# Optimization experiments

Measured on AMD Instinct MI355X. Metric: run time of the kernel, lower is better.

Reference implementation:

```python
import jax, jax.numpy as jnp
import numpy as np

NODE_DIM = 128
DEPTH = 4
N_NODES = 10000
N_EDGES = 320000


def setup_inputs() -> dict:
    key = jax.random.key(0)
    ks = jax.random.split(key, 12)
    s = 0.05
    D = NODE_DIM
    inp = {
        'h': jax.random.normal(ks[0], (N_NODES, D), jnp.float32),
        'x': jax.random.normal(ks[1], (N_NODES, 3), jnp.float32),
        'edges': jax.random.randint(ks[2], (2, N_EDGES), 0, N_NODES, jnp.int32),
        # edge_mlp: Linear(2D+1 -> D), SiLU, Linear(D -> D), SiLU  (per layer)
        'edge_w1': jax.random.normal(ks[3], (DEPTH, 2 * D + 1, D), jnp.float32) * s,
        'edge_b1': jnp.zeros((DEPTH, D), jnp.float32),
        'edge_w2': jax.random.normal(ks[4], (DEPTH, D, D), jnp.float32) * s,
        'edge_b2': jnp.zeros((DEPTH, D), jnp.float32),
        # node_mlp: Linear(2D -> D), SiLU, Linear(D -> D)  (per layer)
        'node_w1': jax.random.normal(ks[5], (DEPTH, 2 * D, D), jnp.float32) * s,
        'node_b1': jnp.zeros((DEPTH, D), jnp.float32),
        'node_w2': jax.random.normal(ks[6], (DEPTH, D, D), jnp.float32) * s,
        'node_b2': jnp.zeros((DEPTH, D), jnp.float32),
        # coord_mlp (only used by last layer, update_coords=True):
        # Linear(D -> D), SiLU, Linear(D -> 1, bias=False)
        'coord_w1': jax.random.normal(ks[7], (D, D), jnp.float32) * s,
        'coord_b1': jnp.zeros((D,), jnp.float32),
        'coord_w2': jax.random.normal(ks[8], (D, 1), jnp.float32) * s,
    }
    return inp


def reference(h, x, edges, edge_w1, edge_b1, edge_w2, edge_b2,
              node_w1, node_b1, node_w2, node_b2,
              coord_w1, coord_b1, coord_w2):
    silu = jax.nn.silu
    row, col = edges[0], edges[1]
    n = h.shape[0]
    for i in range(DEPTH):
        # coord2radial
        coord_diff = x[row] - x[col]                       # [E, 3]
        radial = jnp.sum(coord_diff * coord_diff, axis=-1, keepdims=True)  # [E, 1]
        # edge_model: m_ij = edge_mlp([h_i, h_j, radial])
        feat = jnp.concatenate([h[row], h[col], radial], axis=-1)  # [E, 2D+1]
        m = silu(feat @ edge_w1[i] + edge_b1[i])
        m = silu(m @ edge_w2[i] + edge_b2[i])              # [E, D]
        # coord_model (only last layer, coords_agg='mean')
        if i == DEPTH - 1:
            w = silu(m @ coord_w1 + coord_b1) @ coord_w2   # [E, 1]
            trans = coord_diff * w                          # [E, 3]
            agg = jax.ops.segment_sum(trans, row, num_segments=n)
            cnt = jax.ops.segment_sum(jnp.ones((row.shape[0], 1), trans.dtype),
                                      row, num_segments=n)
            x = x + agg / jnp.maximum(cnt, 1.0)
        # node_model: h = h + node_mlp([h, sum_j m_ij])  (residual=True)
        magg = jax.ops.segment_sum(m, row, num_segments=n)  # [N, D]
        hin = jnp.concatenate([h, magg], axis=-1)           # [N, 2D]
        out = silu(hin @ node_w1[i] + node_b1[i]) @ node_w2[i] + node_b2[i]
        h = h + out
    return h, x
```

## Files before the change

### kernel.cpp

```cpp
#include <hip/hip_runtime.h>

#define NND 10000
#define NE  320000
#define DD  128
#define NDEPTH 4
#define TE  128

typedef __attribute__((ext_vector_type(8))) short s8b;
typedef __attribute__((ext_vector_type(4))) float f4;
typedef unsigned short u16;
typedef unsigned int   u32;

__device__ __forceinline__ u16 f2b(float f) {
    u32 u = __builtin_bit_cast(u32, f);
    u32 r = (u + 0x7fffu + ((u >> 16) & 1u)) >> 16;
    return (u16)r;
}

__device__ __forceinline__ float b2f(u16 b) {
    u32 u = (u32)b << 16;
    return __builtin_bit_cast(float, u);
}

__device__ __forceinline__ u32 cvt_pk(float lo, float hi) {
    u32 r;
    asm("v_cvt_pk_bf16_f32 %0, %1, %2" : "=v"(r) : "v"(lo), "v"(hi));
    return r;
}

__device__ __forceinline__ float silu_f(float v) {
    return v / (1.0f + __expf(-v));
}

__device__ __forceinline__ s8b frag_a(const u16* rowp, int g) {
    union { s8b v; uint2 u2[2]; } r;
    r.u2[0] = *(const uint2*)(rowp + 4 * g);
    r.u2[1] = *(const uint2*)(rowp + 16 + 4 * g);
    return r.v;
}

__device__ __forceinline__ f4 mfma16(s8b a, s8b b, f4 c) {
    return __builtin_amdgcn_mfma_f32_16x16x32_bf16(a, b, c, 0, 0, 0);
}

__global__ __launch_bounds__(256) void egnn_pack(
    const float* __restrict__ ew1, const float* __restrict__ ew2,
    const float* __restrict__ nw1, const float* __restrict__ nw2,
    const float* __restrict__ cw1, u16* __restrict__ pw)
{
    int t = blockIdx.x * 256 + threadIdx.x;
    if (t >= 25 * 16384) return;
    int mat = t >> 14;
    int r   = t & 16383;
    int kt  = r >> 12;
    int nt  = (r >> 9) & 7;
    int lane= (r >> 3) & 63;
    int j   = r & 7;
    int g = lane >> 4, l15 = lane & 15;
    int k = kt * 32 + ((j < 4) ? (4 * g + j) : (16 + 4 * g + (j - 4)));
    int n = nt * 16 + l15;
    float v;
    if (mat < 24) {
        int layer = mat / 6, tp = mat % 6;
        switch (tp) {
            case 0: v = ew1[((size_t)layer * 257 + k) * DD + n]; break;
            case 1: v = ew1[((size_t)layer * 257 + 128 + k) * DD + n]; break;
            case 2: v = ew2[((size_t)layer * 128 + k) * DD + n]; break;
            case 3: v = nw1[((size_t)layer * 256 + k) * DD + n]; break;
            case 4: v = nw1[((size_t)layer * 256 + 128 + k) * DD + n]; break;
            default: v = nw2[((size_t)layer * 128 + k) * DD + n]; break;
        }
    } else {
        v = cw1[(size_t)k * DD + n];
    }
    pw[t] = f2b(v);
}

__global__ __launch_bounds__(256) void egnn_init(
    const float* __restrict__ h, u16* __restrict__ hb)
{
    int i = blockIdx.x * 256 + threadIdx.x;
    size_t base = (size_t)i * 4;
    if (base >= (size_t)NND * DD) return;
    float4 v = *(const float4*)(h + base);
    union { u16 s[4]; uint2 u; } t2;
    t2.s[0] = f2b(v.x); t2.s[1] = f2b(v.y); t2.s[2] = f2b(v.z); t2.s[3] = f2b(v.w);
    *(uint2*)(hb + base) = t2.u;
}

__global__ __launch_bounds__(256) void egnn_count(
    const int* __restrict__ edges, int* __restrict__ cnts)
{
    int e = blockIdx.x * 256 + threadIdx.x;
    if (e < NE) atomicAdd(&cnts[edges[e]], 1);
}

__global__ __launch_bounds__(1024) void egnn_scan(
    const int* __restrict__ cnts, int* __restrict__ off, int* __restrict__ cursor)
{
    __shared__ int part[1024];
    const int t = threadIdx.x;
    const int base = t * 10;
    int s = 0;
    #pragma unroll
    for (int j = 0; j < 10; ++j) {
        int i = base + j;
        s += (i < NND) ? cnts[i] : 0;
    }
    part[t] = s;
    __syncthreads();
    for (int d = 1; d < 1024; d <<= 1) {
        int v = (t >= d) ? part[t - d] : 0;
        __syncthreads();
        part[t] += v;
        __syncthreads();
    }
    int run = (t == 0) ? 0 : part[t - 1];
    #pragma unroll
    for (int j = 0; j < 10; ++j) {
        int i = base + j;
        if (i <= NND) { off[i] = run; cursor[i] = run; }
        if (i < NND) run += cnts[i];
    }
}

__global__ __launch_bounds__(256) void egnn_scatter(
    const int* __restrict__ edges, int* __restrict__ cursor,
    int* __restrict__ perm, int* __restrict__ rowsorted)
{
    int e = blockIdx.x * 256 + threadIdx.x;
    if (e >= NE) return;
    int r = edges[e];
    int p = atomicAdd(&cursor[r], 1);
    perm[p] = e;
    rowsorted[p] = r;
}

__global__ __launch_bounds__(256) void egnn_pre0(
    const u16* __restrict__ hb, const u16* __restrict__ pw,
    float* __restrict__ Pb, float* __restrict__ Qb)
{
    __shared__ __attribute__((aligned(16))) u16 tH[64][136];
    const int tid = threadIdx.x;
    const int n0  = blockIdx.x * 64;

    #pragma unroll
    for (int it = 0; it < 4; ++it) {
        int idx = tid + it * 256;
        int el = idx >> 4, part = idx & 15;
        int node = n0 + el;
        if (node < NND) {
            *(uint4*)&tH[el][part * 8] = *(const uint4*)(hb + (size_t)node * DD + part * 8);
        } else {
            uint4 z = {0u, 0u, 0u, 0u};
            *(uint4*)&tH[el][part * 8] = z;
        }
    }
    __syncthreads();

    const int wv = tid >> 6, lane = tid & 63;
    const int g = lane >> 4, l15 = lane & 15;
    const int wrow = wv * 16;

    f4 accP[8], accQ[8];
    #pragma unroll
    for (int nt = 0; nt < 8; ++nt) { accP[nt] = f4{0.f,0.f,0.f,0.f}; accQ[nt] = f4{0.f,0.f,0.f,0.f}; }
    const u16* pwa = pw;
    const u16* pwb = pw + 16384;
    #pragma unroll
    for (int kt = 0; kt < 4; ++kt) {
        s8b a = frag_a(&tH[wrow + l15][kt * 32], g);
        const u16* ba = pwa + (size_t)kt * 4096 + lane * 8;
        const u16* bb = pwb + (size_t)kt * 4096 + lane * 8;
        #pragma unroll
        for (int nt = 0; nt < 8; ++nt) {
            accP[nt] = mfma16(a, *(const s8b*)(ba + nt * 512), accP[nt]);
            accQ[nt] = mfma16(a, *(const s8b*)(bb + nt * 512), accQ[nt]);
        }
    }
    #pragma unroll
    for (int nt = 0; nt < 8; ++nt) {
        int n = nt * 16 + l15;
        #pragma unroll
        for (int r = 0; r < 4; ++r) {
            int node = n0 + wrow + g * 4 + r;
            if (node < NND) {
                Pb[(size_t)node * DD + n] = accP[nt][r];
                Qb[(size_t)node * DD + n] = accQ[nt][r];
            }
        }
    }
}

__global__ __launch_bounds__(256, 4) void egnn_edge(
    const float* __restrict__ Pb, const float* __restrict__ Qb,
    const float* __restrict__ xin,
    const int* __restrict__ edges,
    const int* __restrict__ perm, const int* __restrict__ rowsorted,
    const u16* __restrict__ pw,
    const float* __restrict__ ew1, const float* __restrict__ eb1,
    const float* __restrict__ eb2, const float* __restrict__ cb1,
    const float* __restrict__ cw2,
    float* __restrict__ magg, float* __restrict__ aggx,
    int layer, int last)
{
    __shared__ __attribute__((aligned(16))) u16 tA[TE][136];
    __shared__ float rad[TE];
    __shared__ float cdf[TE][3];
    __shared__ int   ridx[TE];
    __shared__ int   cidx[TE];
    __shared__ unsigned char segflag[TE + 1];

    const int tid = threadIdx.x;
    const int p0  = blockIdx.x * TE;

    if (tid < TE) {
        int p = p0 + tid;
        int e = perm[p];
        int r = rowsorted[p];
        int c = edges[NE + e];
        ridx[tid] = r; cidx[tid] = c;
        float d0 = xin[r * 3 + 0] - xin[c * 3 + 0];
        float d1 = xin[r * 3 + 1] - xin[c * 3 + 1];
        float d2 = xin[r * 3 + 2] - xin[c * 3 + 2];
        rad[tid] = d0 * d0 + d1 * d1 + d2 * d2;
        cdf[tid][0] = d0; cdf[tid][1] = d1; cdf[tid][2] = d2;
    }
    __syncthreads();

    if (tid < TE) {
        segflag[tid] = (tid == 0) || (ridx[tid] != ridx[tid - 1]);
        if (tid == 0) segflag[TE] = 1;
    }

    {
        const int cg = tid & 15;
        const int rg = tid >> 4;
        const float* b1p = eb1 + (size_t)layer * DD + cg * 8;
        const float* wrp = ew1 + ((size_t)layer * 257 + 256) * DD + cg * 8;
        float4 b0 = *(const float4*)(b1p);
        float4 b4 = *(const float4*)(b1p + 4);
        float4 w0 = *(const float4*)(wrp);
        float4 w4 = *(const float4*)(wrp + 4);
        #pragma unroll
        for (int k = 0; k < 8; ++k) {
            int row = rg + 16 * k;
            int rn = ridx[row], cn = cidx[row];
            float rd = rad[row];
            const float* pp = Pb + (size_t)rn * DD + cg * 8;
            const float* qq = Qb + (size_t)cn * DD + cg * 8;
            float4 pa = *(const float4*)(pp);
            float4 pc = *(const float4*)(pp + 4);
            float4 qa = *(const float4*)(qq);
            float4 qc = *(const float4*)(qq + 4);
            float v0 = silu_f(pa.x + qa.x + b0.x + rd * w0.x);
            float v1 = silu_f(pa.y + qa.y + b0.y + rd * w0.y);
            float v2 = silu_f(pa.z + qa.z + b0.z + rd * w0.z);
            float v3 = silu_f(pa.w + qa.w + b0.w + rd * w0.w);
            float v4 = silu_f(pc.x + qc.x + b4.x + rd * w4.x);
            float v5 = silu_f(pc.y + qc.y + b4.y + rd * w4.y);
            float v6 = silu_f(pc.z + qc.z + b4.z + rd * w4.z);
            float v7 = silu_f(pc.w + qc.w + b4.w + rd * w4.w);
            union { u32 w[4]; uint4 u; } cv;
            cv.w[0] = cvt_pk(v0, v1);
            cv.w[1] = cvt_pk(v2, v3);
            cv.w[2] = cvt_pk(v4, v5);
            cv.w[3] = cvt_pk(v6, v7);
            *(uint4*)&tA[row][cg * 8] = cv.u;
        }
    }
    __syncthreads();

    const int wv = tid >> 6, lane = tid & 63;
    const int g = lane >> 4, l15 = lane & 15;
    const int wrow = wv * 32;

    f4 acc2[2][8];
    #pragma unroll
    for (int mi = 0; mi < 2; ++mi)
        #pragma unroll
        for (int nt = 0; nt < 8; ++nt) acc2[mi][nt] = f4{0.f, 0.f, 0.f, 0.f};
    const u16* pw2 = pw + (size_t)(layer * 6 + 2) * 16384;
    #pragma unroll
    for (int kt = 0; kt < 4; ++kt) {
        const int k0 = kt * 32;
        s8b a0 = frag_a(&tA[wrow + l15][k0], g);
        s8b a1 = frag_a(&tA[wrow + 16 + l15][k0], g);
        const u16* pb = pw2 + (size_t)kt * 4096 + lane * 8;
        #pragma unroll
        for (int nt = 0; nt < 8; ++nt) {
            s8b b = *(const s8b*)(pb + nt * 512);
            acc2[0][nt] = mfma16(a0, b, acc2[0][nt]);
            acc2[1][nt] = mfma16(a1, b, acc2[1][nt]);
        }
    }
    {
        const float* b2 = eb2 + (size_t)layer * DD;
        #pragma unroll
        for (int nt = 0; nt < 8; ++nt) {
            int n = nt * 16 + l15;
            float bb = b2[n];
            #pragma unroll
            for (int mi = 0; mi < 2; ++mi)
                #pragma unroll
                for (int r = 0; r < 4; ++r) {
                    int er = wrow + mi * 16 + g * 4 + r;
                    float v = silu_f(acc2[mi][nt][r] + bb);
                    tA[er][n] = f2b(v);
                }
        }
    }
    __syncthreads();

    {
        int col  = tid & 127;
        int half = tid >> 7;
        int r0 = half * 64, r1 = r0 + 64;
        float s = 0.f;
        for (int row = r0; row < r1; ++row) {
            s += b2f(tA[row][col]);
            if (segflag[row + 1] || row == r1 - 1) {
                atomicAdd(&magg[(size_t)ridx[row] * DD + col], s);
                s = 0.f;
            }
        }
    }

    if (last) {
        f4 acc3[2][8];
        #pragma unroll
        for (int mi = 0; mi < 2; ++mi)
            #pragma unroll
            for (int nt = 0; nt < 8; ++nt) acc3[mi][nt] = f4{0.f, 0.f, 0.f, 0.f};
        const u16* pwc = pw + (size_t)24 * 16384;
        #pragma unroll
        for (int kt = 0; kt < 4; ++kt) {
            const int k0 = kt * 32;
            s8b a0 = frag_a(&tA[wrow + l15][k0], g);
            s8b a1 = frag_a(&tA[wrow + 16 + l15][k0], g);
            const u16* pb = pwc + (size_t)kt * 4096 + lane * 8;
            #pragma unroll
            for (int nt = 0; nt < 8; ++nt) {
                s8b b = *(const s8b*)(pb + nt * 512);
                acc3[0][nt] = mfma16(a0, b, acc3[0][nt]);
                acc3[1][nt] = mfma16(a1, b, acc3[1][nt]);
            }
        }
        float p[2][4];
        #pragma unroll
        for (int mi = 0; mi < 2; ++mi)
            #pragma unroll
            for (int r = 0; r < 4; ++r) p[mi][r] = 0.f;
        #pragma unroll
        for (int nt = 0; nt < 8; ++nt) {
            int n = nt * 16 + l15;
            float bb = cb1[n], w2 = cw2[n];
            #pragma unroll
            for (int mi = 0; mi < 2; ++mi)
                #pragma unroll
                for (int r = 0; r < 4; ++r)
                    p[mi][r] += silu_f(acc3[mi][nt][r] + bb) * w2;
        }
        #pragma unroll
        for (int off = 1; off < 16; off <<= 1) {
            #pragma unroll
            for (int mi = 0; mi < 2; ++mi)
                #pragma unroll
                for (int r = 0; r < 4; ++r)
                    p[mi][r] += __shfl_xor(p[mi][r], off);
        }
        if (l15 == 0) {
            #pragma unroll
            for (int mi = 0; mi < 2; ++mi)
                #pragma unroll
                for (int r = 0; r < 4; ++r) {
                    int er = wrow + mi * 16 + 4 * g + r;
                    int rn = ridx[er];
                    float w = p[mi][r];
                    atomicAdd(&aggx[rn * 3 + 0], cdf[er][0] * w);
                    atomicAdd(&aggx[rn * 3 + 1], cdf[er][1] * w);
                    atomicAdd(&aggx[rn * 3 + 2], cdf[er][2] * w);
                }
        }
    }
}

__global__ __launch_bounds__(256) void egnn_node(
    const u16* __restrict__ hb, const float* __restrict__ resid,
    const float* __restrict__ magg, const u16* __restrict__ pw,
    const float* __restrict__ nb1, const float* __restrict__ nb2,
    float* __restrict__ out_h, u16* __restrict__ hb_out,
    float* __restrict__ Pb, float* __restrict__ Qb,
    int layer, int last)
{
    __shared__ __attribute__((aligned(16))) u16 tH[64][136];
    __shared__ __attribute__((aligned(16))) u16 tM[64][136];
    const int tid = threadIdx.x;
    const int n0  = blockIdx.x * 64;

    #pragma unroll
    for (int it = 0; it < 4; ++it) {
        int idx = tid + it * 256;
        int el = idx >> 4, part = idx & 15;
        int node = n0 + el;
        if (node < NND) {
            *(uint4*)&tH[el][part * 8] = *(const uint4*)(hb + (size_t)node * DD + part * 8);
            const float* ms = magg + (size_t)node * DD + part * 8;
            float4 m0 = *(const float4*)(ms);
            float4 m1 = *(const float4*)(ms + 4);
            union { u32 w[4]; uint4 u; } cv;
            cv.w[0] = cvt_pk(m0.x, m0.y);
            cv.w[1] = cvt_pk(m0.z, m0.w);
            cv.w[2] = cvt_pk(m1.x, m1.y);
            cv.w[3] = cvt_pk(m1.z, m1.w);
            *(uint4*)&tM[el][part * 8] = cv.u;
        } else {
            uint4 z = {0u, 0u, 0u, 0u};
            *(uint4*)&tH[el][part * 8] = z;
            *(uint4*)&tM[el][part * 8] = z;
        }
    }
    __syncthreads();

    const int wv = tid >> 6, lane = tid & 63;
    const int g = lane >> 4, l15 = lane & 15;
    const int wrow = wv * 16;

    f4 acc[8];
    #pragma unroll
    for (int nt = 0; nt < 8; ++nt) acc[nt] = f4{0.f, 0.f, 0.f, 0.f};
    const u16* pn1a = pw + (size_t)(layer * 6 + 3) * 16384;
    const u16* pn1b = pw + (size_t)(layer * 6 + 4) * 16384;
    #pragma unroll
    for (int kt = 0; kt < 8; ++kt) {
        const u16 (*tile)[136] = (kt < 4) ? tH : tM;
        const int k0 = (kt & 3) * 32;
        s8b a = frag_a(&tile[wrow + l15][k0], g);
        const u16* pb = ((kt < 4) ? pn1a : pn1b) + (size_t)(kt & 3) * 4096 + lane * 8;
        #pragma unroll
        for (int nt = 0; nt < 8; ++nt) {
            s8b b = *(const s8b*)(pb + nt * 512);
            acc[nt] = mfma16(a, b, acc[nt]);
        }
    }
    {
        const float* b1 = nb1 + (size_t)layer * DD;
        #pragma unroll
        for (int nt = 0; nt < 8; ++nt) {
            int n = nt * 16 + l15;
            float bb = b1[n];
            #pragma unroll
            for (int r = 0; r < 4; ++r) {
                int er = wrow + g * 4 + r;
                tM[er][n] = f2b(silu_f(acc[nt][r] + bb));
            }
        }
    }
    __syncthreads();

    f4 acc2[8];
    #pragma unroll
    for (int nt = 0; nt < 8; ++nt) acc2[nt] = f4{0.f, 0.f, 0.f, 0.f};
    const u16* pn2 = pw + (size_t)(layer * 6 + 5) * 16384;
    #pragma unroll
    for (int kt = 0; kt < 4; ++kt) {
        s8b a = frag_a(&tM[wrow + l15][kt * 32], g);
        const u16* pb = pn2 + (size_t)kt * 4096 + lane * 8;
        #pragma unroll
        for (int nt = 0; nt < 8; ++nt) {
            s8b b = *(const s8b*)(pb + nt * 512);
            acc2[nt] = mfma16(a, b, acc2[nt]);
        }
    }
    {
        const float* b2 = nb2 + (size_t)layer * DD;
        #pragma unroll
        for (int nt = 0; nt < 8; ++nt) {
            int n = nt * 16 + l15;
            float bb = b2[n];
            #pragma unroll
            for (int r = 0; r < 4; ++r) {
                int er = wrow + g * 4 + r;
                int node = n0 + er;
                if (node < NND) {
                    float v = acc2[nt][r] + bb + resid[(size_t)node * DD + n];
                    out_h[(size_t)node * DD + n] = v;
                    if (!last) {
                        u16 hv = f2b(v);
                        hb_out[(size_t)node * DD + n] = hv;
                        tH[er][n] = hv;
                    }
                } else if (!last) {
                    tH[er][n] = 0;
                }
            }
        }
    }

    if (!last) {
        __syncthreads();
        f4 accP[8], accQ[8];
        #pragma unroll
        for (int nt = 0; nt < 8; ++nt) { accP[nt] = f4{0.f,0.f,0.f,0.f}; accQ[nt] = f4{0.f,0.f,0.f,0.f}; }
        const u16* pwa = pw + (size_t)((layer + 1) * 6 + 0) * 16384;
        const u16* pwb = pw + (size_t)((layer + 1) * 6 + 1) * 16384;
        #pragma unroll
        for (int kt = 0; kt < 4; ++kt) {
            s8b a = frag_a(&tH[wrow + l15][kt * 32], g);
            const u16* ba = pwa + (size_t)kt * 4096 + lane * 8;
            const u16* bb = pwb + (size_t)kt * 4096 + lane * 8;
            #pragma unroll
            for (int nt = 0; nt < 8; ++nt) {
                accP[nt] = mfma16(a, *(const s8b*)(ba + nt * 512), accP[nt]);
                accQ[nt] = mfma16(a, *(const s8b*)(bb + nt * 512), accQ[nt]);
            }
        }
        #pragma unroll
        for (int nt = 0; nt < 8; ++nt) {
            int n = nt * 16 + l15;
            #pragma unroll
            for (int r = 0; r < 4; ++r) {
                int node = n0 + wrow + g * 4 + r;
                if (node < NND) {
                    Pb[(size_t)node * DD + n] = accP[nt][r];
                    Qb[(size_t)node * DD + n] = accQ[nt][r];
                }
            }
        }
    }
}

__global__ __launch_bounds__(256) void egnn_coord_out(
    const float* __restrict__ xin, const float* __restrict__ aggx,
    const int* __restrict__ off, float* __restrict__ out_x)
{
    int i = blockIdx.x * 256 + threadIdx.x;
    if (i >= NND) return;
    float c = (float)(off[i + 1] - off[i]);
    float inv = 1.0f / fmaxf(c, 1.0f);
    out_x[i * 3 + 0] = xin[i * 3 + 0] + aggx[i * 3 + 0] * inv;
    out_x[i * 3 + 1] = xin[i * 3 + 1] + aggx[i * 3 + 1] * inv;
    out_x[i * 3 + 2] = xin[i * 3 + 2] + aggx[i * 3 + 2] * inv;
}

extern "C" void kernel_launch(void* const* d_in, const int* in_sizes, int n_in,
                              void* d_out, int out_size, void* d_ws, size_t ws_size,
                              hipStream_t stream) {
    const float* h   = (const float*)d_in[0];
    const float* x   = (const float*)d_in[1];
    const int*  edges= (const int*)d_in[2];
    const float* ew1 = (const float*)d_in[3];
    const float* eb1 = (const float*)d_in[4];
    const float* ew2 = (const float*)d_in[5];
    const float* eb2 = (const float*)d_in[6];
    const float* nw1 = (const float*)d_in[7];
    const float* nb1 = (const float*)d_in[8];
    const float* nw2 = (const float*)d_in[9];
    const float* nb2 = (const float*)d_in[10];
    const float* cw1 = (const float*)d_in[11];
    const float* cb1 = (const float*)d_in[12];
    const float* cw2 = (const float*)d_in[13];

    char* ws = (char*)d_ws;
    u16*   hb   = (u16*)  (ws);
    float* magg = (float*)(ws + 2560000);
    float* aggx = (float*)(ws + 7680000);
    u16*   pw   = (u16*)  (ws + 7800064);
    int*   cnts = (int*)  (ws + 8619264);
    int*   off  = (int*)  (ws + 8659280);
    int*   curs = (int*)  (ws + 8699296);
    int*   perm = (int*)  (ws + 8739312);
    int*   rows = (int*)  (ws + 10019312);
    float* Pb   = (float*)(ws + 11299312);
    float* Qb   = (float*)(ws + 16419312);

    float* out_h = (float*)d_out;
    float* out_x = out_h + (size_t)NND * DD;

    egnn_pack<<<1600, 256, 0, stream>>>(ew1, ew2, nw1, nw2, cw1, pw);
    egnn_init<<<1250, 256, 0, stream>>>(h, hb);
    hipMemsetAsync(aggx, 0, 120064, stream);
    hipMemsetAsync(cnts, 0, 40016, stream);

    egnn_count<<<1250, 256, 0, stream>>>(edges, cnts);
    egnn_scan<<<1, 1024, 0, stream>>>(cnts, off, curs);
    egnn_scatter<<<1250, 256, 0, stream>>>(edges, curs, perm, rows);
    egnn_pre0<<<(NND + 63) / 64, 256, 0, stream>>>(hb, pw, Pb, Qb);

    for (int i = 0; i < NDEPTH; ++i) {
        int last = (i == NDEPTH - 1);
        hipMemsetAsync(magg, 0, (size_t)NND * DD * 4, stream);
        egnn_edge<<<NE / TE, 256, 0, stream>>>(Pb, Qb, x, edges, perm, rows, pw,
                                               ew1, eb1, eb2, cb1, cw2,
                                               magg, aggx, i, last);
        const float* resid = (i == 0) ? h : (const float*)out_h;
        egnn_node<<<(NND + 63) / 64, 256, 0, stream>>>(hb, resid, magg, pw, nb1, nb2,
                                                       out_h, hb, Pb, Qb, i, last);
    }
    egnn_coord_out<<<40, 256, 0, stream>>>(x, aggx, off, out_x);
}
```

Measured before the change: 561.3 us.

## Halve edge tile to 64 edges per block and raise edge kernel occupancy

Shrinks the edge-kernel tile from 128 to 64 edges, so each wave computes one 16-row MFMA slab instead of two, and raises launch bounds to 6 blocks per CU. The segmented reduction into magg is restructured so each thread sums two columns over a 16-row slice, instead of one column over 64 rows. The aim is to cut register and LDS use per block for more concurrency and latency hiding on the gathers. The cost is twice as many blocks, each with less reuse of the weight fragments per loaded B operand, and more segment boundaries, which means more atomics.

```diff
diff --git a/kernel.cpp b/kernel.cpp
--- a/kernel.cpp
+++ b/kernel.cpp
@@ -4,7 +4,7 @@
 #define NE  320000
 #define DD  128
 #define NDEPTH 4
-#define TE  128
+#define TE  64
 
 typedef __attribute__((ext_vector_type(8))) short s8b;
 typedef __attribute__((ext_vector_type(4))) float f4;
@@ -192,7 +192,7 @@
     }
 }
 
-__global__ __launch_bounds__(256, 4) void egnn_edge(
+__global__ __launch_bounds__(256, 6) void egnn_edge(
     const float* __restrict__ Pb, const float* __restrict__ Qb,
     const float* __restrict__ xin,
     const int* __restrict__ edges,
@@ -243,7 +243,7 @@
         float4 w0 = *(const float4*)(wrp);
         float4 w4 = *(const float4*)(wrp + 4);
         #pragma unroll
-        for (int k = 0; k < 8; ++k) {
+        for (int k = 0; k < 4; ++k) {
             int row = rg + 16 * k;
             int rn = ridx[row], cn = cidx[row];
             float rd = rad[row];
@@ -273,25 +273,20 @@
 
     const int wv = tid >> 6, lane = tid & 63;
     const int g = lane >> 4, l15 = lane & 15;
-    const int wrow = wv * 32;
-
-    f4 acc2[2][8];
-    #pragma unroll
-    for (int mi = 0; mi < 2; ++mi)
-        #pragma unroll
-        for (int nt = 0; nt < 8; ++nt) acc2[mi][nt] = f4{0.f, 0.f, 0.f, 0.f};
+    const int wrow = wv * 16;
+
+    f4 acc2[8];
+    #pragma unroll
+    for (int nt = 0; nt < 8; ++nt) acc2[nt] = f4{0.f, 0.f, 0.f, 0.f};
     const u16* pw2 = pw + (size_t)(layer * 6 + 2) * 16384;
     #pragma unroll
     for (int kt = 0; kt < 4; ++kt) {
-        const int k0 = kt * 32;
-        s8b a0 = frag_a(&tA[wrow + l15][k0], g);
-        s8b a1 = frag_a(&tA[wrow + 16 + l15][k0], g);
+        s8b a = frag_a(&tA[wrow + l15][kt * 32], g);
         const u16* pb = pw2 + (size_t)kt * 4096 + lane * 8;
         #pragma unroll
         for (int nt = 0; nt < 8; ++nt) {
             s8b b = *(const s8b*)(pb + nt * 512);
-            acc2[0][nt] = mfma16(a0, b, acc2[0][nt]);
-            acc2[1][nt] = mfma16(a1, b, acc2[1][nt]);
+            acc2[nt] = mfma16(a, b, acc2[nt]);
         }
     }
     {
@@ -301,86 +296,76 @@
             int n = nt * 16 + l15;
             float bb = b2[n];
             #pragma unroll
-            for (int mi = 0; mi < 2; ++mi)
-                #pragma unroll
-                for (int r = 0; r < 4; ++r) {
-                    int er = wrow + mi * 16 + g * 4 + r;
-                    float v = silu_f(acc2[mi][nt][r] + bb);
-                    tA[er][n] = f2b(v);
-                }
+            for (int r = 0; r < 4; ++r) {
+                int er = wrow + g * 4 + r;
+                float v = silu_f(acc2[nt][r] + bb);
+                tA[er][n] = f2b(v);
+            }
         }
     }
     __syncthreads();
 
     {
-        int col  = tid & 127;
-        int half = tid >> 7;
-        int r0 = half * 64, r1 = r0 + 64;
-        float s = 0.f;
-        for (int row = r0; row < r1; ++row) {
-            s += b2f(tA[row][col]);
-            if (segflag[row + 1] || row == r1 - 1) {
-                atomicAdd(&magg[(size_t)ridx[row] * DD + col], s);
-                s = 0.f;
+        int cg2 = tid & 63;
+        int r0  = wv * 16;
+        float s0 = 0.f, s1 = 0.f;
+        #pragma unroll
+        for (int i = 0; i < 16; ++i) {
+            int row = r0 + i;
+            u32 v = *(const u32*)&tA[row][cg2 * 2];
+            s0 += b2f((u16)(v & 0xffffu));
+            s1 += b2f((u16)(v >> 16));
+            if (segflag[row + 1] || i == 15) {
+                float* mg = &magg[(size_t)ridx[row] * DD + cg2 * 2];
+                atomicAdd(mg, s0);
+                atomicAdd(mg + 1, s1);
+                s0 = 0.f; s1 = 0.f;
             }
         }
     }
 
     if (last) {
-        f4 acc3[2][8];
-        #pragma unroll
-        for (int mi = 0; mi < 2; ++mi)
-            #pragma unroll
-            for (int nt = 0; nt < 8; ++nt) acc3[mi][nt] = f4{0.f, 0.f, 0.f, 0.f};
+        f4 acc3[8];
+        #pragma unroll
+        for (int nt = 0; nt < 8; ++nt) acc3[nt] = f4{0.f, 0.f, 0.f, 0.f};
         const u16* pwc = pw + (size_t)24 * 16384;
         #pragma unroll
         for (int kt = 0; kt < 4; ++kt) {
-            const int k0 = kt * 32;
-            s8b a0 = frag_a(&tA[wrow + l15][k0], g);
-            s8b a1 = frag_a(&tA[wrow + 16 + l15][k0], g);
+            s8b a = frag_a(&tA[wrow + l15][kt * 32], g);
             const u16* pb = pwc + (size_t)kt * 4096 + lane * 8;
             #pragma unroll
             for (int nt = 0; nt < 8; ++nt) {
                 s8b b = *(const s8b*)(pb + nt * 512);
-                acc3[0][nt] = mfma16(a0, b, acc3[0][nt]);
-                acc3[1][nt] = mfma16(a1, b, acc3[1][nt]);
-            }
-        }
-        float p[2][4];
-        #pragma unroll
-        for (int mi = 0; mi < 2; ++mi)
-            #pragma unroll
-            for (int r = 0; r < 4; ++r) p[mi][r] = 0.f;
+                acc3[nt] = mfma16(a, b, acc3[nt]);
+            }
+        }
+        float p[4];
+        #pragma unroll
+        for (int r = 0; r < 4; ++r) p[r] = 0.f;
         #pragma unroll
         for (int nt = 0; nt < 8; ++nt) {
             int n = nt * 16 + l15;
             float bb = cb1[n], w2 = cw2[n];
             #pragma unroll
-            for (int mi = 0; mi < 2; ++mi)
-                #pragma unroll
-                for (int r = 0; r < 4; ++r)
-                    p[mi][r] += silu_f(acc3[mi][nt][r] + bb) * w2;
+            for (int r = 0; r < 4; ++r)
+                p[r] += silu_f(acc3[nt][r] + bb) * w2;
         }
         #pragma unroll
         for (int off = 1; off < 16; off <<= 1) {
             #pragma unroll
-            for (int mi = 0; mi < 2; ++mi)
-                #pragma unroll
-                for (int r = 0; r < 4; ++r)
-                    p[mi][r] += __shfl_xor(p[mi][r], off);
+            for (int r = 0; r < 4; ++r)
+                p[r] += __shfl_xor(p[r], off);
         }
         if (l15 == 0) {
             #pragma unroll
-            for (int mi = 0; mi < 2; ++mi)
-                #pragma unroll
-                for (int r = 0; r < 4; ++r) {
-                    int er = wrow + mi * 16 + 4 * g + r;
-                    int rn = ridx[er];
-                    float w = p[mi][r];
-                    atomicAdd(&aggx[rn * 3 + 0], cdf[er][0] * w);
-                    atomicAdd(&aggx[rn * 3 + 1], cdf[er][1] * w);
-                    atomicAdd(&aggx[rn * 3 + 2], cdf[er][2] * w);
-                }
+            for (int r = 0; r < 4; ++r) {
+                int er = wrow + 4 * g + r;
+                int rn = ridx[er];
+                float w = p[r];
+                atomicAdd(&aggx[rn * 3 + 0], cdf[er][0] * w);
+                atomicAdd(&aggx[rn * 3 + 1], cdf[er][1] * w);
+                atomicAdd(&aggx[rn * 3 + 2], cdf[er][2] * w);
+            }
         }
     }
 }
```

Result: slower. 573.4 us (+2.1%).
